# Kernel optimization log

Hardware: AMD Instinct MI355X
Metric: run time of the kernel (lower is better)

Reference implementation:

```python
import jax, jax.numpy as jnp
import numpy as np

B, T, H, NH, DH, R = 2, 2048, 1024, 16, 64, 256
ALPHA = 0.6


def setup_inputs() -> dict:
    key = jax.random.key(0)
    ks = jax.random.split(key, 28)
    f32 = jnp.float32

    def nrm(k, shape, s=0.02):
        return jax.random.normal(k, shape, dtype=f32) * s

    inp = {}
    inp['x'] = jax.random.normal(ks[0], (B, T, H), dtype=f32)
    # additive causal mask [1,1,T,T]: 0 on/below diagonal, -1e9 above
    causal = jnp.tril(jnp.ones((T, T), dtype=bool))
    inp['attention_mask'] = jnp.where(causal, 0.0, -1e9).astype(f32)[None, None]
    # low-rank SVD factors for q,k,v,o: Vh [H,R], S [R] (positive), U [H,R], b [H]
    i = 1
    for name in ('q', 'k', 'v', 'o'):
        inp['Vh_' + name] = nrm(ks[i], (H, R)); i += 1
        inp['S_' + name] = jax.random.uniform(ks[i], (R,), dtype=f32, minval=0.5, maxval=1.5); i += 1
        inp['U_' + name] = nrm(ks[i], (H, R)); i += 1
        inp['b_' + name] = jnp.zeros((H,), dtype=f32); i += 1
    # full-rank weights of the original (fallback) attention: y = x @ W + b (Conv1D style)
    for name in ('q', 'k', 'v', 'o'):
        inp['W_' + name] = nrm(ks[i], (H, H)); i += 1
        inp['bf_' + name] = jnp.zeros((H,), dtype=f32); i += 1
    return inp


def _split_heads(t):
    # [B,T,H] -> [B,nH,T,dH]
    Bs, Ts, _ = t.shape
    return t.reshape(Bs, Ts, NH, DH).transpose(0, 2, 1, 3)


def _attention(Q, K, V, mask):
    q, k, v = _split_heads(Q), _split_heads(K), _split_heads(V)
    scores = jnp.einsum('bhtd,bhsd->bhts', q, k) / (DH ** 0.5)
    scores = scores + mask
    w = jax.nn.softmax(scores, axis=-1)
    ctx = jnp.einsum('bhts,bhsd->bhtd', w, v)
    Bs = ctx.shape[0]
    return ctx.transpose(0, 2, 1, 3).reshape(Bs, -1, NH * DH)


def _lowrank(x, Vh, S, U, b):
    # ((x @ Vh) * S) @ U.T + b
    return ((x @ Vh) * S) @ U.T + b


def reference(x, attention_mask,
              Vh_q, S_q, U_q, b_q, Vh_k, S_k, U_k, b_k,
              Vh_v, S_v, U_v, b_v, Vh_o, S_o, U_o, b_o,
              W_q, bf_q, W_k, bf_k, W_v, bf_v, W_o, bf_o):
    # --- low-rank SVD path ---
    Q = _lowrank(x, Vh_q, S_q, U_q, b_q)
    K = _lowrank(x, Vh_k, S_k, U_k, b_k)
    V = _lowrank(x, Vh_v, S_v, U_v, b_v)
    ctx = _attention(Q, K, V, attention_mask)
    out = _lowrank(ctx, Vh_o, S_o, U_o, b_o)
    # --- fallback: original full-rank attention ---
    Qf = x @ W_q + bf_q
    Kf = x @ W_k + bf_k
    Vf = x @ W_v + bf_v
    ctxf = _attention(Qf, Kf, Vf, attention_mask)
    fallback_out = ctxf @ W_o + bf_o
    return ALPHA * out + (1.0 - ALPHA) * fallback_out
```

## Files before the change

kernel.cpp:

```cpp
#include <hip/hip_runtime.h>
#include <hip/hip_bf16.h>

typedef __bf16 bf16_t;
typedef __bf16 bf16x8 __attribute__((ext_vector_type(8)));
typedef float f32x4 __attribute__((ext_vector_type(4)));
typedef _Float16 f16_t;
typedef _Float16 f16x4 __attribute__((ext_vector_type(4)));

extern "C" __device__ float __ocml_native_exp2_f32(float);

#define DEVI static __device__ __forceinline__

static constexpr int TN   = 2048;
static constexpr int Hn   = 1024;
static constexpr int Rn   = 256;
static constexpr int MTOK = 4096;
static constexpr int NCAT = 6144;

static constexpr float QSCALE = 0.125f;
static constexpr float LOG2E  = 1.44269504088896340736f;
static constexpr float SOFT_OFF2 = 0.426950408889634f;

template <typename T>
DEVI void gload16(const T* g, T* l) {
    __builtin_amdgcn_global_load_lds(
        (const __attribute__((address_space(1))) void*)g,
        (__attribute__((address_space(3))) void*)l, 16, 0, 0);
}

DEVI float loadf(const void* base, int idx, bool bfm) {
    if (bfm) {
        unsigned int u = ((const unsigned short*)base)[idx];
        u <<= 16;
        return __builtin_bit_cast(float, u);
    }
    return ((const float*)base)[idx];
}
DEVI bool detect_bf16(const void* mask) {
    return fabsf(((const float*)mask)[0]) > 1.0f;
}

struct PrepArgs {
    const void *x, *mask;
    const void *Vh[4], *S[4], *U[4];
    const void *bb[4], *bfb[4];
    bf16_t *Xb, *Abuf, *Bbuf;
    float *biascat, *biaso;
};

__global__ void k_prep(PrepArgs a) {
    const bool bfm = detect_bf16(a.mask);
    const int bid = blockIdx.x;
    if (bid < 4096) {
        int i = (bid * 256 + threadIdx.x) * 4;
#pragma unroll
        for (int j = 0; j < 4; ++j) a.Xb[i + j] = (bf16_t)loadf(a.x, i + j, bfm);
    } else if (bid < 8192) {
        int idx = (bid - 4096) * 256 + threadIdx.x;
        int proj = idx >> 18;
        int e = idx & 262143;
        int r = e & 255;
        float s = loadf(a.S[proj], r, bfm);
        if (proj == 0) s *= QSCALE * LOG2E;
        if (proj == 3) s *= 0.6f;
        a.Abuf[idx] = (bf16_t)(loadf(a.U[proj], e, bfm) * s);
        a.Bbuf[idx] = (bf16_t)loadf(a.Vh[proj], e, bfm);
    } else {
        int i = (bid - 8192) * 256 + threadIdx.x;
        if (i < 1024)      a.biascat[i] = QSCALE * LOG2E * loadf(a.bb[0], i, bfm);
        else if (i < 2048) a.biascat[i] = loadf(a.bb[1], i - 1024, bfm);
        else if (i < 3072) a.biascat[i] = loadf(a.bb[2], i - 2048, bfm);
        else if (i < 4096) a.biascat[i] = QSCALE * LOG2E * loadf(a.bfb[0], i - 3072, bfm);
        else if (i < 5120) a.biascat[i] = loadf(a.bfb[1], i - 4096, bfm);
        else if (i < 6144) a.biascat[i] = loadf(a.bfb[2], i - 5120, bfm);
        else {
            int j = i - 6144;
            a.biaso[j] = 0.6f * loadf(a.bb[3], j, bfm) + 0.4f * loadf(a.bfb[3], j, bfm);
        }
    }
}

struct TransP { const void* W[4]; bf16_t* dst[4]; int ldd[4]; float scale[4]; const void* mask; };

__global__ void k_transpose4(TransP tp) {
    const bool bfm = detect_bf16(tp.mask);
    const int z = blockIdx.z;
    const void* W = tp.W[z];
    bf16_t* dst = tp.dst[z];
    const int ldd = tp.ldd[z];
    const float scale = tp.scale[z];
    __shared__ float t[32][33];
    int bx = blockIdx.x * 32, by = blockIdx.y * 32;
    int tx = threadIdx.x, ty = threadIdx.y;
#pragma unroll
    for (int k = 0; k < 32; k += 8)
        t[ty + k][tx] = loadf(W, (by + ty + k) * Hn + bx + tx, bfm);
    __syncthreads();
#pragma unroll
    for (int k = 0; k < 32; k += 8)
        dst[(size_t)(bx + ty + k) * ldd + by + tx] = (bf16_t)(scale * t[tx][ty + k]);
}

template <int MI>
DEVI void gemm_core64(const bf16_t* __restrict__ A, int lda,
                      const bf16_t* __restrict__ B, int ldb, int K,
                      bf16_t* A0, bf16_t* A1, bf16_t* B0, bf16_t* B1,
                      int bm, int bn, f32x4 (&acc)[MI][4]) {
    constexpr int MT = MI * 32;
    const int tid  = threadIdx.x;
    const int lane = tid & 63;
    const int w    = tid >> 6;
    const int wr   = (w >> 1) * (MI * 16);
    const int wc   = (w & 1) * 64;
    const int fr   = lane & 15;
    const int quad = lane >> 4;

#pragma unroll
    for (int i = 0; i < MI; ++i)
#pragma unroll
        for (int j = 0; j < 4; ++j) acc[i][j] = {0.f, 0.f, 0.f, 0.f};

    for (int kb = 0; kb < K; kb += 64) {
        __syncthreads();
        for (int u = tid; u < MT * 4; u += 256) {
            const bf16_t* as = &A[(size_t)(bm + (u >> 2)) * lda + kb + (u & 3) * 8];
            gload16(as,      &A0[u * 8]);
            gload16(as + 32, &A1[u * 8]);
        }
#pragma unroll
        for (int t = 0; t < 2; ++t) {
            int u = t * 256 + tid;
            const bf16_t* bs = &B[(size_t)(bn + (u >> 2)) * ldb + kb + (u & 3) * 8];
            gload16(bs,      &B0[u * 8]);
            gload16(bs + 32, &B1[u * 8]);
        }
        __syncthreads();

#pragma unroll
        for (int kk = 0; kk < 2; ++kk) {
            const bf16_t* Ap = kk ? A1 : A0;
            const bf16_t* Bp = kk ? B1 : B0;
            bf16x8 af[MI], bfv[4];
#pragma unroll
            for (int i = 0; i < MI; ++i)
                af[i] = *(const bf16x8*)&Ap[(wr + i * 16 + fr) * 32 + quad * 8];
#pragma unroll
            for (int j = 0; j < 4; ++j)
                bfv[j] = *(const bf16x8*)&Bp[(wc + j * 16 + fr) * 32 + quad * 8];
#pragma unroll
            for (int i = 0; i < MI; ++i)
#pragma unroll
                for (int j = 0; j < 4; ++j)
                    acc[i][j] = __builtin_amdgcn_mfma_f32_16x16x32_bf16(af[i], bfv[j], acc[i][j], 0, 0, 0);
        }
    }
}

template <int MI, bool OUT_DUAL, bool WRITE_VT>
__global__ __launch_bounds__(256)
void k_gemm(const bf16_t* __restrict__ A, int lda,
            const bf16_t* __restrict__ B, int ldb,
            void* __restrict__ C, int ldc, int K,
            const float* __restrict__ bias, const void* __restrict__ mask,
            f16_t* __restrict__ Vt_g) {
    constexpr int MT = MI * 32;
    struct GB { bf16_t A0[MT * 32]; bf16_t A1[MT * 32]; bf16_t B0[4096]; bf16_t B1[4096]; };
    union SM { GB g; f16_t Ls[WRITE_VT ? 128 * 136 : 8]; };
    __shared__ __align__(16) SM sm;

    const int tid  = threadIdx.x;
    const int lane = tid & 63;
    const int w    = tid >> 6;
    const int wr   = (w >> 1) * (MI * 16);
    const int wc   = (w & 1) * 64;
    const int bm   = blockIdx.x * MT;
    const int bn   = blockIdx.y * 128;
    const int fr   = lane & 15;
    const int quad = lane >> 4;

    f32x4 acc[MI][4];
    gemm_core64<MI>(A, lda, B, ldb, K, sm.g.A0, sm.g.A1, sm.g.B0, sm.g.B1, bm, bn, acc);

    if constexpr (WRITE_VT) {
        const bool isV = (bn >= 2048 && bn < 3072) || (bn >= 5120);
        if (isV) {
            const int pth = (bn >= 5120) ? 1 : 0;
            const int colrel = bn - (pth ? 5120 : 2048);
            const int bb = bm >> 11;
            const int R0 = (pth * 32 + bb * 16 + (colrel >> 6)) * 64;
            const int tloc = bm & 2047;
            __syncthreads();
#pragma unroll
            for (int i = 0; i < MI; ++i) {
                const int t0 = wr + i * 16 + quad * 4;
#pragma unroll
                for (int j = 0; j < 4; ++j) {
                    const int c = wc + j * 16 + fr;
                    const float bv = bias[bn + c];
#pragma unroll
                    for (int r = 0; r < 4; ++r)
                        sm.Ls[c * 136 + t0 + r] = (f16_t)(acc[i][j][r] + bv);
                }
            }
            __syncthreads();
            const int c = tid >> 1, seg = tid & 1;
            f16_t* dst = &Vt_g[(size_t)(R0 + c) * TN + tloc + seg * 64];
            const f16_t* src = &sm.Ls[c * 136 + seg * 64];
#pragma unroll
            for (int e = 0; e < 8; ++e)
                *(uint4*)&dst[e * 8] = *(const uint4*)&src[e * 8];
            return;
        }
    }

    bool bfm = false;
    if constexpr (OUT_DUAL) bfm = detect_bf16(mask);
#pragma unroll
    for (int i = 0; i < MI; ++i) {
        const int row0 = bm + wr + i * 16 + quad * 4;
#pragma unroll
        for (int j = 0; j < 4; ++j) {
            const int col = bn + wc + j * 16 + fr;
            const float bv = bias ? bias[col] : 0.f;
#pragma unroll
            for (int r = 0; r < 4; ++r) {
                float v = acc[i][j][r] + bv;
                size_t ci = (size_t)(row0 + r) * ldc + col;
                if constexpr (OUT_DUAL) {
                    if (bfm) ((unsigned short*)C)[ci] = __builtin_bit_cast(unsigned short, (bf16_t)v);
                    else     ((float*)C)[ci] = v;
                } else {
                    ((bf16_t*)C)[ci] = (bf16_t)v;
                }
            }
        }
    }
}

__global__ __launch_bounds__(512, 2)
void k_gemm8(const bf16_t* __restrict__ A, int lda,
             const bf16_t* __restrict__ B, int ldb,
             bf16_t* __restrict__ C, int ldc, int K,
             const float* __restrict__ bias, f16_t* __restrict__ Vt_g) {
    struct Pipe { bf16_t At[2][2][256 * 32]; bf16_t Bt[2][2][128 * 32]; };
    union SM8 { Pipe p; f16_t Ls[128 * 264]; };
    __shared__ __align__(16) SM8 sm;

    const int tid  = threadIdx.x;
    const int lane = tid & 63;
    const int wid  = tid >> 6;
    const int wr   = (wid >> 1) * 64;
    const int wc   = (wid & 1) * 64;
    const int fr   = lane & 15;
    const int quad = lane >> 4;

    const int bid = blockIdx.x;
    const int sz  = (bid & 7) * 96 + (bid >> 3);
    const int bm  = (sz & 15) * 256;
    const int bn  = (sz >> 4) * 128;

    const int csrc = ((tid & 3) ^ ((tid >> 3) & 3)) * 8;
    const int ksw  = (quad ^ ((fr >> 1) & 3)) * 8;
    const int raB  = (wr + fr) * 32 + ksw;
    const int rbB  = (wc + fr) * 32 + ksw;
    const int r0   = tid >> 2;

    auto stage = [&](int t, int kk) {
        const int bufi = t & 1;
        const int kb = t * 64 + kk * 32;
        gload16(&A[(size_t)(bm + r0) * lda + kb + csrc],       &sm.p.At[bufi][kk][tid * 8]);
        gload16(&A[(size_t)(bm + 128 + r0) * lda + kb + csrc], &sm.p.At[bufi][kk][(512 + tid) * 8]);
        gload16(&B[(size_t)(bn + r0) * ldb + kb + csrc],       &sm.p.Bt[bufi][kk][tid * 8]);
    };

    f32x4 acc[4][4];
#pragma unroll
    for (int i = 0; i < 4; ++i)
#pragma unroll
        for (int j = 0; j < 4; ++j) acc[i][j] = {0.f, 0.f, 0.f, 0.f};

    const int NT = K >> 6;
    stage(0, 0);
    stage(0, 1);

    for (int t = 0; t < NT; ++t) {
        const int cur = t & 1;
#pragma unroll
        for (int kk = 0; kk < 2; ++kk) {
            if (t + 1 < NT) {
                stage(t + 1, kk);
                asm volatile("s_waitcnt vmcnt(6)" ::: "memory");
            } else if (kk == 0) {
                asm volatile("s_waitcnt vmcnt(3)" ::: "memory");
            } else {
                asm volatile("s_waitcnt vmcnt(0)" ::: "memory");
            }
            __builtin_amdgcn_s_barrier();
            __builtin_amdgcn_sched_barrier(0);

            bf16x8 af[4], bv[4];
#pragma unroll
            for (int i = 0; i < 4; ++i)
                af[i] = *(const bf16x8*)&sm.p.At[cur][kk][raB + i * 512];
#pragma unroll
            for (int j = 0; j < 4; ++j)
                bv[j] = *(const bf16x8*)&sm.p.Bt[cur][kk][rbB + j * 512];

            __builtin_amdgcn_s_setprio(1);
#pragma unroll
            for (int i = 0; i < 4; ++i)
#pragma unroll
                for (int j = 0; j < 4; ++j)
                    acc[i][j] = __builtin_amdgcn_mfma_f32_16x16x32_bf16(af[i], bv[j], acc[i][j], 0, 0, 0);
            __builtin_amdgcn_s_setprio(0);
        }
    }

    const bool isV = (bn >= 2048 && bn < 3072) || (bn >= 5120);
    if (isV) {
        const int pth = (bn >= 5120) ? 1 : 0;
        const int pbase = pth ? 5120 : 2048;
        const int bb = bm >> 11;
        const int vrow0 = (pth * 32 + bb * 16) * 64 + (bn - pbase);
        const int tloc = bm & 2047;
        __syncthreads();
#pragma unroll
        for (int j = 0; j < 4; ++j) {
            const int c = wc + j * 16 + fr;
            const float bv = bias[bn + c];
#pragma unroll
            for (int i = 0; i < 4; ++i) {
                const int t0 = wr + i * 16 + quad * 4;
                f16x4 pk;
#pragma unroll
                for (int r = 0; r < 4; ++r) pk[r] = (f16_t)(acc[i][j][r] + bv);
                *(f16x4*)&sm.Ls[c * 264 + t0] = pk;
            }
        }
        __syncthreads();
        const int c = tid >> 2, seg = tid & 3;
        f16_t* dst = &Vt_g[(size_t)(vrow0 + c) * TN + tloc + seg * 64];
        const f16_t* src = &sm.Ls[c * 264 + seg * 64];
#pragma unroll
        for (int e = 0; e < 8; ++e)
            *(uint4*)&dst[e * 8] = *(const uint4*)&src[e * 8];
        return;
    }

#pragma unroll
    for (int i = 0; i < 4; ++i) {
        const int row0 = bm + wr + i * 16 + quad * 4;
#pragma unroll
        for (int j = 0; j < 4; ++j) {
            const int col = bn + wc + j * 16 + fr;
            const float bv = bias[col];
#pragma unroll
            for (int r = 0; r < 4; ++r)
                C[(size_t)(row0 + r) * ldc + col] = (bf16_t)(acc[i][j][r] + bv);
        }
    }
}

__global__ __launch_bounds__(256)
void k_gemm_small4(const bf16_t* __restrict__ Abuf, const bf16_t* __restrict__ Bbuf,
                   bf16_t* __restrict__ Wcat, bf16_t* __restrict__ WoT) {
    __shared__ __align__(16) bf16_t A0[64 * 32], A1[64 * 32], B0[4096], B1[4096];
    const int z = blockIdx.z;
    const bf16_t* A = Abuf + (size_t)z * Hn * Rn;
    const bf16_t* B = Bbuf + (size_t)z * Hn * Rn;
    bf16_t* C = (z < 3) ? (Wcat + (size_t)z * Hn * Hn) : WoT;
    const int ldc = (z < 3) ? Hn : 2048;

    const int bm = blockIdx.x * 64, bn = blockIdx.y * 128;
    f32x4 acc[2][4];
    gemm_core64<2>(A, Rn, B, Rn, Rn, A0, A1, B0, B1, bm, bn, acc);

    const int lane = threadIdx.x & 63;
    const int w    = threadIdx.x >> 6;
    const int wr   = (w >> 1) * 32;
    const int wc   = (w & 1) * 64;
    const int fr   = lane & 15;
    const int quad = lane >> 4;
#pragma unroll
    for (int i = 0; i < 2; ++i)
#pragma unroll
        for (int j = 0; j < 4; ++j)
#pragma unroll
            for (int r = 0; r < 4; ++r)
                C[(size_t)(bm + wr + i * 16 + quad * 4 + r) * ldc + bn + wc + j * 16 + fr]
                    = (bf16_t)acc[i][j][r];
}

__global__ __launch_bounds__(256, 4)
void k_flash6(const bf16_t* __restrict__ Y, const f16_t* __restrict__ Vt_g,
              bf16_t* __restrict__ Ctx) {
    const int id   = blockIdx.x;
    const int inst = id & 63;
    const int slot = (id >> 6) & 3;
    const int rnd  = id >> 8;
    const int qt2  = (rnd == 0) ? 15 - slot
                   : (rnd == 1) ? 11 - slot
                   : (rnd == 2) ? 4 + slot
                                : slot;
    const int p = inst >> 5, b = (inst >> 4) & 1, h = inst & 15;

    const int tid  = threadIdx.x;
    const int lane = tid & 63;
    const int w    = tid >> 6;
    const int fr   = lane & 15;
    const int quad = lane >> 4;

    const int rowbase = b * TN;
    const int qbase   = qt2 * 128;
    const int qcol = p * 3072 + h * 64;
    const int kcol = qcol + 1024;
    const int ccol = p * 1024 + h * 64;

    __shared__ __align__(16) bf16_t Kb[2][2][64 * 32];
    __shared__ __align__(16) f16_t  Vb[2][64 * 64];

    const int r64 = tid >> 2;
    const int c8s = (((tid & 3) ^ ((tid >> 4) & 3)) * 8);
    const int ksw = (quad ^ ((fr >> 2) & 3)) * 8;

    size_t vsrc[2];
#pragma unroll
    for (int t = 0; t < 2; ++t) {
        int pp = w * 128 + t * 64 + lane;
        int d  = pp >> 3;
        vsrc[t] = (size_t)(inst * 64 + d) * TN + ((((pp & 7) - d) & 7) * 8);
    }

    f16x4 ones;
#pragma unroll
    for (int j = 0; j < 4; ++j) ones[j] = (f16_t)1.0f;

    const f32x4 off4 = {-SOFT_OFF2, -SOFT_OFF2, -SOFT_OFF2, -SOFT_OFF2};

    bf16x8 qf[2][2];
#pragma unroll
    for (int s = 0; s < 2; ++s) {
        const size_t qrow = (size_t)(rowbase + qbase + s * 64 + w * 16 + fr) * NCAT + qcol;
        qf[s][0] = *(const bf16x8*)&Y[qrow + quad * 8];
        qf[s][1] = *(const bf16x8*)&Y[qrow + 32 + quad * 8];
    }

    f32x4 o[2][4], lacc[2];
#pragma unroll
    for (int s = 0; s < 2; ++s) {
        lacc[s] = {0.f, 0.f, 0.f, 0.f};
#pragma unroll
        for (int db = 0; db < 4; ++db) o[s][db] = {0.f, 0.f, 0.f, 0.f};
    }

    const int t0 = (quad >> 1) + (fr & 7);
    const int h4 = (quad & 1) * 4;
    int voff[4];
#pragma unroll
    for (int nb = 0; nb < 4; ++nb) voff[nb] = ((nb * 2 + t0) & 7) * 8;

    const int kl = quad * 4;
    const int ql = w * 16 + fr;

    const int kmax = 2 * qt2 + 1;

    auto stage = [&](int kt, int bsel) {
        const bf16_t* ksrc = &Y[(size_t)(rowbase + kt * 64 + r64) * NCAT + kcol + c8s];
        gload16(ksrc,      &Kb[bsel][0][tid * 8]);
        gload16(ksrc + 32, &Kb[bsel][1][tid * 8]);
#pragma unroll
        for (int t = 0; t < 2; ++t)
            gload16(&Vt_g[vsrc[t] + kt * 64], &Vb[bsel][(w * 128 + t * 64 + lane) * 8]);
    };

    stage(0, 0);

    for (int kt = 0; kt <= kmax; ++kt) {
        const int cur = kt & 1;
        __syncthreads();
        if (kt < kmax) stage(kt + 1, cur ^ 1);

        const bool a0 = (kt < kmax);

        f16x4 pf[2][4];
#pragma unroll
        for (int nb = 0; nb < 4; ++nb) {
            const int ka = (nb * 16 + fr) * 32 + ksw;
            bf16x8 kf0 = *(const bf16x8*)&Kb[cur][0][ka];
            bf16x8 kf1 = *(const bf16x8*)&Kb[cur][1][ka];
#pragma unroll
            for (int s = 0; s < 2; ++s) {
                if (s == 0 && !a0) continue;
                f32x4 t4 = __builtin_amdgcn_mfma_f32_16x16x32_bf16(kf0, qf[s][0], off4, 0, 0, 0);
                t4 = __builtin_amdgcn_mfma_f32_16x16x32_bf16(kf1, qf[s][1], t4, 0, 0, 0);
                if (kt == 2 * qt2 + s) {
#pragma unroll
                    for (int r = 0; r < 4; ++r)
                        if (nb * 16 + kl + r > ql) t4[r] = -1e30f;
                }
                auto lo = __builtin_amdgcn_cvt_pkrtz(__ocml_native_exp2_f32(t4[0]),
                                                     __ocml_native_exp2_f32(t4[1]));
                auto hi = __builtin_amdgcn_cvt_pkrtz(__ocml_native_exp2_f32(t4[2]),
                                                     __ocml_native_exp2_f32(t4[3]));
                pf[s][nb] = __builtin_bit_cast(f16x4, __builtin_shufflevector(lo, hi, 0, 1, 2, 3));
            }
        }

#pragma unroll
        for (int s = 0; s < 2; ++s) {
            if (s == 0 && !a0) continue;
#pragma unroll
            for (int nb = 0; nb < 4; ++nb)
                lacc[s] = __builtin_amdgcn_mfma_f32_16x16x16f16(pf[s][nb], ones, lacc[s], 0, 0, 0);
        }

#pragma unroll
        for (int db = 0; db < 4; ++db) {
            const int vbase = (db * 16 + fr) * 64 + h4;
            f16x4 vf[4];
#pragma unroll
            for (int nb = 0; nb < 4; ++nb)
                vf[nb] = *(const f16x4*)&Vb[cur][vbase + voff[nb]];
#pragma unroll
            for (int nb = 0; nb < 4; ++nb) {
                o[1][db] = __builtin_amdgcn_mfma_f32_16x16x16f16(pf[1][nb], vf[nb], o[1][db], 0, 0, 0);
                if (a0)
                    o[0][db] = __builtin_amdgcn_mfma_f32_16x16x16f16(pf[0][nb], vf[nb], o[0][db], 0, 0, 0);
            }
        }
    }

#pragma unroll
    for (int s = 0; s < 2; ++s)
#pragma unroll
        for (int r = 0; r < 4; ++r) {
            const float inv = 1.0f / lacc[s][r];
            const size_t trow = (size_t)(rowbase + qbase + s * 64 + w * 16 + quad * 4 + r);
#pragma unroll
            for (int db = 0; db < 4; ++db)
                Ctx[trow * 2048 + ccol + db * 16 + fr] = (bf16_t)(o[s][db][r] * inv);
        }
}

extern "C" void kernel_launch(void* const* d_in, const int* in_sizes, int n_in,
                              void* d_out, int out_size, void* d_ws, size_t ws_size,
                              hipStream_t stream) {
    const void* x    = d_in[0];
    const void* mask = d_in[1];
    const void* Vh[4] = { d_in[2],  d_in[6],  d_in[10], d_in[14] };
    const void* Sp[4] = { d_in[3],  d_in[7],  d_in[11], d_in[15] };
    const void* Up[4] = { d_in[4],  d_in[8],  d_in[12], d_in[16] };
    const void* bb[4] = { d_in[5],  d_in[9],  d_in[13], d_in[17] };
    const void* Wp[4] = { d_in[18], d_in[20], d_in[22], d_in[24] };
    const void* bf[4] = { d_in[19], d_in[21], d_in[23], d_in[25] };

    char* ws = (char*)d_ws;
    size_t off = 0;
    auto alloc = [&](size_t bytes) -> void* {
        void* p = ws + off;
        off = (off + bytes + 255) & ~(size_t)255;
        return p;
    };
    bf16_t* Xb      = (bf16_t*)alloc((size_t)MTOK * Hn * 2);
    bf16_t* Wcat    = (bf16_t*)alloc((size_t)NCAT * Hn * 2);
    bf16_t* Yb      = (bf16_t*)alloc((size_t)MTOK * NCAT * 2);
    bf16_t* Ctx     = (bf16_t*)alloc((size_t)MTOK * 2048 * 2);
    bf16_t* WoT     = (bf16_t*)alloc((size_t)Hn * 2048 * 2);
    f16_t*  Vt_g    = (f16_t*)alloc((size_t)64 * 64 * TN * 2);
    bf16_t* Abuf    = (bf16_t*)alloc((size_t)4 * Hn * Rn * 2);
    bf16_t* Bbuf    = (bf16_t*)alloc((size_t)4 * Hn * Rn * 2);
    float*  biascat = (float*)alloc(NCAT * 4);
    float*  biaso   = (float*)alloc(Hn * 4);

    PrepArgs pa;
    pa.x = x; pa.mask = mask;
    for (int i = 0; i < 4; ++i) {
        pa.Vh[i] = Vh[i]; pa.S[i] = Sp[i]; pa.U[i] = Up[i];
        pa.bb[i] = bb[i]; pa.bfb[i] = bf[i];
    }
    pa.Xb = Xb; pa.Abuf = Abuf; pa.Bbuf = Bbuf; pa.biascat = biascat; pa.biaso = biaso;
    k_prep<<<8220, 256, 0, stream>>>(pa);

    TransP tp;
    for (int i = 0; i < 3; ++i) {
        tp.W[i] = Wp[i]; tp.dst[i] = Wcat + (size_t)(3 * Hn + i * Hn) * Hn;
        tp.ldd[i] = Hn; tp.scale[i] = (i == 0) ? QSCALE * LOG2E : 1.0f;
    }
    tp.W[3] = Wp[3]; tp.dst[3] = WoT + 1024; tp.ldd[3] = 2048; tp.scale[3] = 0.4f;
    tp.mask = mask;
    k_transpose4<<<dim3(32, 32, 4), dim3(32, 8), 0, stream>>>(tp);

    k_gemm_small4<<<dim3(16, 8, 4), 256, 0, stream>>>(Abuf, Bbuf, Wcat, WoT);

    k_gemm8<<<768, 512, 0, stream>>>(
        Xb, Hn, Wcat, Hn, Yb, NCAT, Hn, biascat, Vt_g);

    k_flash6<<<1024, 256, 0, stream>>>(Yb, Vt_g, Ctx);

    k_gemm<2, true, false><<<dim3(64, 8), 256, 0, stream>>>(
        Ctx, 2048, WoT, 2048, d_out, Hn, 2048, biaso, mask, nullptr);
}
```

Baseline: 308.6 us.

## Use 4-slot ring buffer with 3-deep prefetch in fused projection GEMM

Replaces the double-buffered two-substage K pipeline with a four-slot ring of 32-wide K slices, so three slices are in flight ahead of compute. A second barrier per step protects the slot being overwritten. The block-index swizzle that grouped blocks for L2 locality is also dropped in favour of plain row-major tiling. The deeper prefetch targets exposed global-load latency, at the cost of an extra barrier per slice and possibly worse cache reuse across blocks.

```diff
diff --git a/kernel.cpp b/kernel.cpp
--- a/kernel.cpp
+++ b/kernel.cpp
@@ -242,7 +242,7 @@
              const bf16_t* __restrict__ B, int ldb,
              bf16_t* __restrict__ C, int ldc, int K,
              const float* __restrict__ bias, f16_t* __restrict__ Vt_g) {
-    struct Pipe { bf16_t At[2][2][256 * 32]; bf16_t Bt[2][2][128 * 32]; };
+    struct Pipe { bf16_t At[4][256 * 32]; bf16_t Bt[4][128 * 32]; };
     union SM8 { Pipe p; f16_t Ls[128 * 264]; };
     __shared__ __align__(16) SM8 sm;
 
@@ -255,9 +255,8 @@
     const int quad = lane >> 4;
 
     const int bid = blockIdx.x;
-    const int sz  = (bid & 7) * 96 + (bid >> 3);
-    const int bm  = (sz & 15) * 256;
-    const int bn  = (sz >> 4) * 128;
+    const int bm  = (bid & 15) * 256;
+    const int bn  = (bid >> 4) * 128;
 
     const int csrc = ((tid & 3) ^ ((tid >> 3) & 3)) * 8;
     const int ksw  = (quad ^ ((fr >> 1) & 3)) * 8;
@@ -265,12 +264,12 @@
     const int rbB  = (wc + fr) * 32 + ksw;
     const int r0   = tid >> 2;
 
-    auto stage = [&](int t, int kk) {
-        const int bufi = t & 1;
-        const int kb = t * 64 + kk * 32;
-        gload16(&A[(size_t)(bm + r0) * lda + kb + csrc],       &sm.p.At[bufi][kk][tid * 8]);
-        gload16(&A[(size_t)(bm + 128 + r0) * lda + kb + csrc], &sm.p.At[bufi][kk][(512 + tid) * 8]);
-        gload16(&B[(size_t)(bn + r0) * ldb + kb + csrc],       &sm.p.Bt[bufi][kk][tid * 8]);
+    auto stage = [&](int sidx) {
+        const int slot = sidx & 3;
+        const int kb = sidx * 32;
+        gload16(&A[(size_t)(bm + r0) * lda + kb + csrc],       &sm.p.At[slot][tid * 8]);
+        gload16(&A[(size_t)(bm + 128 + r0) * lda + kb + csrc], &sm.p.At[slot][(512 + tid) * 8]);
+        gload16(&B[(size_t)(bn + r0) * ldb + kb + csrc],       &sm.p.Bt[slot][tid * 8]);
     };
 
     f32x4 acc[4][4];
@@ -279,41 +278,42 @@
 #pragma unroll
         for (int j = 0; j < 4; ++j) acc[i][j] = {0.f, 0.f, 0.f, 0.f};
 
-    const int NT = K >> 6;
-    stage(0, 0);
-    stage(0, 1);
-
-    for (int t = 0; t < NT; ++t) {
-        const int cur = t & 1;
-#pragma unroll
-        for (int kk = 0; kk < 2; ++kk) {
-            if (t + 1 < NT) {
-                stage(t + 1, kk);
-                asm volatile("s_waitcnt vmcnt(6)" ::: "memory");
-            } else if (kk == 0) {
-                asm volatile("s_waitcnt vmcnt(3)" ::: "memory");
-            } else {
-                asm volatile("s_waitcnt vmcnt(0)" ::: "memory");
-            }
-            __builtin_amdgcn_s_barrier();
-            __builtin_amdgcn_sched_barrier(0);
-
-            bf16x8 af[4], bv[4];
-#pragma unroll
-            for (int i = 0; i < 4; ++i)
-                af[i] = *(const bf16x8*)&sm.p.At[cur][kk][raB + i * 512];
+    const int NS = K >> 5;
+    stage(0); stage(1); stage(2);
+
+    for (int s = 0; s < NS; ++s) {
+        if (s + 3 < NS) {
+            stage(s + 3);
+            asm volatile("s_waitcnt vmcnt(9)" ::: "memory");
+        } else if (s + 3 == NS) {
+            asm volatile("s_waitcnt vmcnt(6)" ::: "memory");
+        } else if (s + 2 == NS) {
+            asm volatile("s_waitcnt vmcnt(3)" ::: "memory");
+        } else {
+            asm volatile("s_waitcnt vmcnt(0)" ::: "memory");
+        }
+        __builtin_amdgcn_s_barrier();
+        __builtin_amdgcn_sched_barrier(0);
+
+        const int slot = s & 3;
+        bf16x8 af[4], bv[4];
+#pragma unroll
+        for (int i = 0; i < 4; ++i)
+            af[i] = *(const bf16x8*)&sm.p.At[slot][raB + i * 512];
+#pragma unroll
+        for (int j = 0; j < 4; ++j)
+            bv[j] = *(const bf16x8*)&sm.p.Bt[slot][rbB + j * 512];
+
+        __builtin_amdgcn_s_setprio(1);
+#pragma unroll
+        for (int i = 0; i < 4; ++i)
 #pragma unroll
             for (int j = 0; j < 4; ++j)
-                bv[j] = *(const bf16x8*)&sm.p.Bt[cur][kk][rbB + j * 512];
-
-            __builtin_amdgcn_s_setprio(1);
-#pragma unroll
-            for (int i = 0; i < 4; ++i)
-#pragma unroll
-                for (int j = 0; j < 4; ++j)
-                    acc[i][j] = __builtin_amdgcn_mfma_f32_16x16x32_bf16(af[i], bv[j], acc[i][j], 0, 0, 0);
-            __builtin_amdgcn_s_setprio(0);
-        }
+                acc[i][j] = __builtin_amdgcn_mfma_f32_16x16x32_bf16(af[i], bv[j], acc[i][j], 0, 0, 0);
+        __builtin_amdgcn_s_setprio(0);
+
+        __builtin_amdgcn_s_barrier();
+        __builtin_amdgcn_sched_barrier(0);
     }
 
     const bool isV = (bn >= 2048 && bn < 3072) || (bn >= 5120);
```

After: 304.7 us. Within noise of the previous version (-1.3%).
